# Kernel tuning notes

Measured on AMD Instinct MI355X. Metric: run time of the kernel, lower is better.

## Reference

```python
import jax, jax.numpy as jnp
import numpy as np

B = 256
N = 256


def setup_inputs() -> dict:
    key = jax.random.key(0)
    ks = jax.random.split(key, 6)
    X = jax.random.normal(ks[0], (B, N), dtype=jnp.float32)
    context = jax.random.normal(ks[1], (B, N), dtype=jnp.float32)
    W = jax.random.normal(ks[2], (N, N), dtype=jnp.float32) * 0.1
    scale = jnp.ones((1,), dtype=jnp.float32)
    A = jax.random.uniform(ks[3], (N, N), dtype=jnp.float32)
    cl_weight = jax.random.normal(ks[4], (N * N, N), dtype=jnp.float32) * 0.02
    cl_bias = jax.random.normal(ks[5], (N * N,), dtype=jnp.float32) * 0.02
    t = 3
    return {"X": X, "context": context, "W": W, "scale": scale, "A": A,
            "cl_weight": cl_weight, "cl_bias": cl_bias, "t": t}


def reference(X, context, W, scale, A, cl_weight, cl_bias, t):
    # context_L path: context-conditioned adjustment of W, shape [B, N, N]
    Bsz, n = X.shape
    adjust = (context @ cl_weight.T + cl_bias).reshape(Bsz, n, n)
    W_new = adjust + W  # broadcast [N,N] over batch
    # diag term: sum over rows i of (W_new @ A)[b, i, k] = einsum bij,jk->bk
    d = jnp.einsum('bij,jk->bk', W_new, A)
    eye = jnp.eye(n, dtype=X.dtype)
    L = d[:, :, None] * eye - W_new          # diag_embed(d) - W_new, [B,N,N]
    new_context = context * (t / (t + 1)) + X / (t + 1)
    L_T = scale * jnp.swapaxes(L, -1, -2)    # [B,N,N]
    update = jnp.einsum('bn,bnm->bm', X, L_T)  # matmul(X[...,None,:], L_T).squeeze()
    return (update, new_context)
```

## Files before the change

### kernel.cpp

```cpp
#include <hip/hip_runtime.h>

#define N 256
#define NN 65536

typedef __attribute__((ext_vector_type(8))) __bf16 bf16x8;
typedef __attribute__((ext_vector_type(4))) __bf16 bf16x4v;
typedef __attribute__((ext_vector_type(4))) float f32x4;

#define F_PART   0u
#define F_SPART  2097152u
#define F_WSC    2621440u
#define F_SFULL  2621696u
#define F_YADJ   2687232u
#define WS_FLOATS 2752768u

static __device__ __forceinline__ f32x4 mfma16(bf16x8 a, bf16x8 b, f32x4 c) {
  return __builtin_amdgcn_mfma_f32_16x16x32_bf16(a, b, c, 0, 0, 0);
}
static __device__ __forceinline__ bf16x4v pack4(float4 v) {
  bf16x4v r;
  r[0] = (__bf16)v.x; r[1] = (__bf16)v.y; r[2] = (__bf16)v.z; r[3] = (__bf16)v.w;
  return r;
}
static __device__ __forceinline__ bf16x8 pack8(float4 a, float4 b) {
  bf16x8 r;
  r[0] = (__bf16)a.x; r[1] = (__bf16)a.y; r[2] = (__bf16)a.z; r[3] = (__bf16)a.w;
  r[4] = (__bf16)b.x; r[5] = (__bf16)b.y; r[6] = (__bf16)b.z; r[7] = (__bf16)b.w;
  return r;
}

__global__ void __launch_bounds__(512) kbig(
    const float* __restrict__ X, const float* __restrict__ ctx,
    const float* __restrict__ W, const float* __restrict__ clb,
    const float* __restrict__ clw, float* __restrict__ ws)
{
  extern __shared__ char smem[];
  float* xl = (float*)(smem + 49152);
  const int t = threadIdx.x;
  const int mt = blockIdx.x >> 5, s = blockIdx.x & 31;
  const int n0 = s * 8, m0g = mt * 32;
  const float4* clwf4 = (const float4*)clw;

  int gm[4], gk[4];
  float4 gA[4], gB[4];
#pragma unroll
  for (int i = 0; i < 4; ++i) {
    const int idx = i * 512 + t;
    gm[i] = idx >> 6; gk[i] = idx & 63;
    gA[i] = clwf4[(m0g + gm[i]) * 16384 + (n0 + 0) * 64 + gk[i]];
  }
#pragma unroll
  for (int i = 0; i < 4; ++i)
    gB[i] = clwf4[(m0g + gm[i]) * 16384 + (n0 + 1) * 64 + gk[i]];

  const int lane = t & 63, w = t >> 6;
  const int wb = w * 32, l15 = lane & 15, lhi = lane >> 4;
  const int swz = (l15 & 7) << 4;

  bf16x8 af[2][8];
#pragma unroll
  for (int i = 0; i < 2; ++i)
#pragma unroll
    for (int c = 0; c < 8; ++c) {
      const float4* p =
          (const float4*)(ctx + (wb + i * 16 + l15) * N + c * 32 + lhi * 8);
      af[i][c] = pack8(p[0], p[1]);
    }

  if (t < 256) {
    const float4* xp = (const float4*)(X + t * N + n0);
    const float4 x0 = xp[0], x1 = xp[1];
    xl[0 * N + t] = x0.x; xl[1 * N + t] = x0.y; xl[2 * N + t] = x0.z; xl[3 * N + t] = x0.w;
    xl[4 * N + t] = x1.x; xl[5 * N + t] = x1.y; xl[6 * N + t] = x1.z; xl[7 * N + t] = x1.w;
  }
#pragma unroll
  for (int i = 0; i < 4; ++i)
    *(bf16x4v*)(smem + gm[i] * 512 + ((gk[i] * 8) ^ ((gm[i] & 7) << 4))) = pack4(gA[i]);
  __syncthreads();

  const f32x4 zero = {0.f, 0.f, 0.f, 0.f};
  f32x4 acc[2][2];
  acc[0][0] = zero; acc[0][1] = zero; acc[1][0] = zero; acc[1][1] = zero;

#pragma unroll
  for (int nn = 0; nn < 8; ++nn) {
    if (nn < 6) {
      if ((nn & 1) == 0) {
#pragma unroll
        for (int i = 0; i < 4; ++i)
          gA[i] = clwf4[(m0g + gm[i]) * 16384 + (n0 + nn + 2) * 64 + gk[i]];
      } else {
#pragma unroll
        for (int i = 0; i < 4; ++i)
          gB[i] = clwf4[(m0g + gm[i]) * 16384 + (n0 + nn + 2) * 64 + gk[i]];
      }
    }
    char* buf = smem + (nn % 3) * 16384;
    f32x4 h[2][2];
    h[0][0] = zero; h[0][1] = zero; h[1][0] = zero; h[1][1] = zero;
#pragma unroll
    for (int c = 0; c < 8; ++c) {
      const int kb = c * 64 + lhi * 16;
      bf16x8 b0 = *(const bf16x8*)(buf + l15 * 512 + (kb ^ swz));
      bf16x8 b1 = *(const bf16x8*)(buf + (16 + l15) * 512 + (kb ^ swz));
      h[0][0] = mfma16(af[0][c], b0, h[0][0]);
      h[0][1] = mfma16(af[0][c], b1, h[0][1]);
      h[1][0] = mfma16(af[1][c], b0, h[1][0]);
      h[1][1] = mfma16(af[1][c], b1, h[1][1]);
    }
    const int ng = n0 + nn;
#pragma unroll
    for (int fb = 0; fb < 2; ++fb) {
#pragma unroll
      for (int r = 0; r < 4; ++r) {
        const float xv = xl[nn * N + wb + fb * 16 + lhi * 4 + r];
        acc[fb][0][r] += xv * h[fb][0][r];
        acc[fb][1][r] += xv * h[fb][1][r];
        float v = h[fb][0][r] + h[fb][1][r];
        v += __shfl_xor(v, 1);
        v += __shfl_xor(v, 2);
        v += __shfl_xor(v, 4);
        v += __shfl_xor(v, 8);
        if (l15 == 0)
          ws[F_SPART + mt * NN + (wb + fb * 16 + lhi * 4 + r) * N + ng] = v;
      }
    }
    if (nn < 7) {
      char* nbuf = smem + ((nn + 1) % 3) * 16384;
      if (((nn + 1) & 1) == 0) {
#pragma unroll
        for (int i = 0; i < 4; ++i)
          *(bf16x4v*)(nbuf + gm[i] * 512 + ((gk[i] * 8) ^ ((gm[i] & 7) << 4))) = pack4(gA[i]);
      } else {
#pragma unroll
        for (int i = 0; i < 4; ++i)
          *(bf16x4v*)(nbuf + gm[i] * 512 + ((gk[i] * 8) ^ ((gm[i] & 7) << 4))) = pack4(gB[i]);
      }
    }
    __syncthreads();
  }
  const int base = blockIdx.x * 8192;
#pragma unroll
  for (int fb = 0; fb < 2; ++fb)
#pragma unroll
    for (int fm = 0; fm < 2; ++fm)
#pragma unroll
      for (int r = 0; r < 4; ++r)
        ws[F_PART + base + (wb + fb * 16 + lhi * 4 + r) * 32 + fm * 16 + l15] =
            acc[fb][fm][r];

  if (mt == 0) {
    float* red = xl;
    if (t < 256) {
      const float4* wp = (const float4*)(W + t * N + s * 8);
      const float4* cp = (const float4*)(clb + t * N + s * 8);
      const float4 a0 = wp[0], a1 = wp[1], b0 = cp[0], b1 = cp[1];
      red[0 * 256 + t] = a0.x + b0.x; red[1 * 256 + t] = a0.y + b0.y;
      red[2 * 256 + t] = a0.z + b0.z; red[3 * 256 + t] = a0.w + b0.w;
      red[4 * 256 + t] = a1.x + b1.x; red[5 * 256 + t] = a1.y + b1.y;
      red[6 * 256 + t] = a1.z + b1.z; red[7 * 256 + t] = a1.w + b1.w;
    }
    __syncthreads();
    if (t < 64) {
      const int jj = t >> 3, seg = t & 7;
      float v = 0.f;
#pragma unroll
      for (int i = 0; i < 32; ++i) v += red[jj * 256 + seg * 32 + i];
      v += __shfl_xor(v, 1);
      v += __shfl_xor(v, 2);
      v += __shfl_xor(v, 4);
      if (seg == 0) ws[F_WSC + s * 8 + jj] = v;
    }
  }
}

__global__ void __launch_bounds__(256) kred(float* __restrict__ ws)
{
  const int o = blockIdx.x * 256 + threadIdx.x;
  const int b = o >> 8, col = o & 255;
  const int mt = col >> 5, ml = col & 31;
  float y = 0.f;
#pragma unroll
  for (int si = 0; si < 32; ++si)
    y += ws[F_PART + ((mt * 32 + si) * 256 + b) * 32 + ml];
  ws[F_YADJ + o] = y;
  float sv = ws[F_WSC + col];
#pragma unroll
  for (int q = 0; q < 8; ++q)
    sv += ws[F_SPART + q * NN + o];
  ws[F_SFULL + o] = sv;
}

__global__ void __launch_bounds__(256) kfin(
    const float* __restrict__ X, const float* __restrict__ ctx,
    const float* __restrict__ W, const float* __restrict__ clb,
    const float* __restrict__ A, const float* __restrict__ scale,
    const int* __restrict__ tptr, float* __restrict__ out,
    float* __restrict__ ws)
{
  extern __shared__ char smem[];
  const int t = threadIdx.x, blk = blockIdx.x;
  const int b0 = (blk >> 3) * 32, k0 = (blk & 7) * 32;
  {
    const int row = t >> 3, q = t & 7;
    const int sw = (row & 7) << 4;
    const float4* sp = (const float4*)(ws + F_SFULL + (b0 + row) * N);
    const float4* xp = (const float4*)(X + (b0 + row) * N);
    const float4* wp = (const float4*)(W + (k0 + row) * N);
    const float4* cp = (const float4*)(clb + (k0 + row) * N);
#pragma unroll
    for (int i = 0; i < 8; ++i) {
      const int f4 = q * 8 + i;
      const int off = row * 512 + ((f4 * 8) ^ sw);
      *(bf16x4v*)(smem + off) = pack4(sp[f4]);
      *(bf16x4v*)(smem + 16384 + off) = pack4(xp[f4]);
      const float4 wv = wp[f4], cv = cp[f4];
      float4 s2;
      s2.x = wv.x + cv.x; s2.y = wv.y + cv.y;
      s2.z = wv.z + cv.z; s2.w = wv.w + cv.w;
      *(bf16x4v*)(smem + 49152 + off) = pack4(s2);
    }
    const float4* ap = (const float4*)(A + t * N + k0);
    char* at = smem + 32768;
#pragma unroll
    for (int i = 0; i < 8; ++i) {
      const float4 v = ap[i];
      const int kk = i * 4;
      *(__bf16*)(at + (kk + 0) * 512 + ((t * 2) ^ (((kk + 0) & 7) << 4))) = (__bf16)v.x;
      *(__bf16*)(at + (kk + 1) * 512 + ((t * 2) ^ (((kk + 1) & 7) << 4))) = (__bf16)v.y;
      *(__bf16*)(at + (kk + 2) * 512 + ((t * 2) ^ (((kk + 2) & 7) << 4))) = (__bf16)v.z;
      *(__bf16*)(at + (kk + 3) * 512 + ((t * 2) ^ (((kk + 3) & 7) << 4))) = (__bf16)v.w;
    }
  }
  __syncthreads();
  const int lane = t & 63, w = t >> 6;
  const int l15 = lane & 15, lhi = lane >> 4;
  const int wqb = (w >> 1) * 16, wqk = (w & 1) * 16;
  const int swz = (l15 & 7) << 4;
  f32x4 accd = {0.f, 0.f, 0.f, 0.f}, accw = {0.f, 0.f, 0.f, 0.f};
#pragma unroll
  for (int c = 0; c < 8; ++c) {
    const int kb = c * 64 + lhi * 16;
    bf16x8 as  = *(const bf16x8*)(smem + (wqb + l15) * 512 + (kb ^ swz));
    bf16x8 aat = *(const bf16x8*)(smem + 32768 + (wqk + l15) * 512 + (kb ^ swz));
    bf16x8 ax  = *(const bf16x8*)(smem + 16384 + (wqb + l15) * 512 + (kb ^ swz));
    bf16x8 awc = *(const bf16x8*)(smem + 49152 + (wqk + l15) * 512 + (kb ^ swz));
    accd = mfma16(as, aat, accd);
    accw = mfma16(ax, awc, accw);
  }
  const float sc = scale[0];
  const float tf = (float)(*tptr);
  const float c1 = tf / (tf + 1.f), c2 = 1.f / (tf + 1.f);
#pragma unroll
  for (int r = 0; r < 4; ++r) {
    const int b = b0 + wqb + lhi * 4 + r, k = k0 + wqk + l15;
    const int idx = b * N + k;
    const float xv = X[idx];
    out[idx] = sc * (xv * accd[r] - accw[r] - ws[F_YADJ + idx]);
    out[NN + idx] = ctx[idx] * c1 + xv * c2;
  }
}

extern "C" void kernel_launch(void* const* d_in, const int* in_sizes, int n_in,
                              void* d_out, int out_size, void* d_ws, size_t ws_size,
                              hipStream_t stream)
{
  (void)in_sizes; (void)n_in; (void)out_size;
  const float* X     = (const float*)d_in[0];
  const float* ctx   = (const float*)d_in[1];
  const float* W     = (const float*)d_in[2];
  const float* scale = (const float*)d_in[3];
  const float* A     = (const float*)d_in[4];
  const float* clw   = (const float*)d_in[5];
  const float* clb   = (const float*)d_in[6];
  const int*   tptr  = (const int*)d_in[7];
  float* out = (float*)d_out;
  float* ws  = (float*)d_ws;

  if (ws_size < (size_t)WS_FLOATS * sizeof(float)) return;

  (void)hipFuncSetAttribute((const void*)kbig,
                            hipFuncAttributeMaxDynamicSharedMemorySize, 57344);
  (void)hipFuncSetAttribute((const void*)kfin,
                            hipFuncAttributeMaxDynamicSharedMemorySize, 65536);

  kbig<<<256, 512, 57344, stream>>>(X, ctx, W, clb, clw, ws);
  kred<<<256, 256, 0, stream>>>(ws);
  kfin<<<64, 256, 65536, stream>>>(X, ctx, W, clb, A, scale, tptr, out, ws);
}
```

Baseline: 55.61 us.

## Deepen clw prefetch to three register stages and stage partial sums in LDS

Moves the global prefetch of cl_weight slices from two to three register buffers, so loads are issued three iterations ahead instead of two. The main loop is hand-unrolled via a macro, and the __syncthreads barriers become a raw s_barrier that only waits on LDS counters, so in-flight global loads are not drained at each step. Per-row scalar stores of the S partial sums now go to an LDS staging area and are written out once at the end as float4 stores. This raises register and LDS use (64KB dynamic shared), which may reduce occupancy.

New measurement: 53.73 us. -3.4%, faster.

```diff
diff --git a/kernel.cpp b/kernel.cpp
--- a/kernel.cpp
+++ b/kernel.cpp
@@ -28,6 +28,11 @@
   r[4] = (__bf16)b.x; r[5] = (__bf16)b.y; r[6] = (__bf16)b.z; r[7] = (__bf16)b.w;
   return r;
 }
+
+#define BAR()                                                  \
+  asm volatile("s_waitcnt lgkmcnt(0)" ::: "memory");           \
+  __builtin_amdgcn_s_barrier();                                \
+  __builtin_amdgcn_sched_barrier(0);
 
 __global__ void __launch_bounds__(512) kbig(
     const float* __restrict__ X, const float* __restrict__ ctx,
@@ -36,22 +41,26 @@
 {
   extern __shared__ char smem[];
   float* xl = (float*)(smem + 49152);
+  float* sred = (float*)(smem + 57344);
   const int t = threadIdx.x;
   const int mt = blockIdx.x >> 5, s = blockIdx.x & 31;
   const int n0 = s * 8, m0g = mt * 32;
   const float4* clwf4 = (const float4*)clw;
 
   int gm[4], gk[4];
-  float4 gA[4], gB[4];
+  float4 g0[4], g1[4], g2[4];
 #pragma unroll
   for (int i = 0; i < 4; ++i) {
     const int idx = i * 512 + t;
     gm[i] = idx >> 6; gk[i] = idx & 63;
-    gA[i] = clwf4[(m0g + gm[i]) * 16384 + (n0 + 0) * 64 + gk[i]];
+    g0[i] = clwf4[(m0g + gm[i]) * 16384 + (n0 + 0) * 64 + gk[i]];
   }
 #pragma unroll
   for (int i = 0; i < 4; ++i)
-    gB[i] = clwf4[(m0g + gm[i]) * 16384 + (n0 + 1) * 64 + gk[i]];
+    g1[i] = clwf4[(m0g + gm[i]) * 16384 + (n0 + 1) * 64 + gk[i]];
+#pragma unroll
+  for (int i = 0; i < 4; ++i)
+    g2[i] = clwf4[(m0g + gm[i]) * 16384 + (n0 + 2) * 64 + gk[i]];
 
   const int lane = t & 63, w = t >> 6;
   const int wb = w * 32, l15 = lane & 15, lhi = lane >> 4;
@@ -75,70 +84,67 @@
   }
 #pragma unroll
   for (int i = 0; i < 4; ++i)
-    *(bf16x4v*)(smem + gm[i] * 512 + ((gk[i] * 8) ^ ((gm[i] & 7) << 4))) = pack4(gA[i]);
-  __syncthreads();
+    *(bf16x4v*)(smem + gm[i] * 512 + ((gk[i] * 8) ^ ((gm[i] & 7) << 4))) = pack4(g0[i]);
+  BAR();
 
   const f32x4 zero = {0.f, 0.f, 0.f, 0.f};
   f32x4 acc[2][2];
   acc[0][0] = zero; acc[0][1] = zero; acc[1][0] = zero; acc[1][1] = zero;
 
-#pragma unroll
-  for (int nn = 0; nn < 8; ++nn) {
-    if (nn < 6) {
-      if ((nn & 1) == 0) {
-#pragma unroll
-        for (int i = 0; i < 4; ++i)
-          gA[i] = clwf4[(m0g + gm[i]) * 16384 + (n0 + nn + 2) * 64 + gk[i]];
-      } else {
-#pragma unroll
-        for (int i = 0; i < 4; ++i)
-          gB[i] = clwf4[(m0g + gm[i]) * 16384 + (n0 + nn + 2) * 64 + gk[i]];
-      }
-    }
-    char* buf = smem + (nn % 3) * 16384;
-    f32x4 h[2][2];
-    h[0][0] = zero; h[0][1] = zero; h[1][0] = zero; h[1][1] = zero;
-#pragma unroll
-    for (int c = 0; c < 8; ++c) {
-      const int kb = c * 64 + lhi * 16;
-      bf16x8 b0 = *(const bf16x8*)(buf + l15 * 512 + (kb ^ swz));
-      bf16x8 b1 = *(const bf16x8*)(buf + (16 + l15) * 512 + (kb ^ swz));
-      h[0][0] = mfma16(af[0][c], b0, h[0][0]);
-      h[0][1] = mfma16(af[0][c], b1, h[0][1]);
-      h[1][0] = mfma16(af[1][c], b0, h[1][0]);
-      h[1][1] = mfma16(af[1][c], b1, h[1][1]);
-    }
-    const int ng = n0 + nn;
-#pragma unroll
-    for (int fb = 0; fb < 2; ++fb) {
-#pragma unroll
-      for (int r = 0; r < 4; ++r) {
-        const float xv = xl[nn * N + wb + fb * 16 + lhi * 4 + r];
-        acc[fb][0][r] += xv * h[fb][0][r];
-        acc[fb][1][r] += xv * h[fb][1][r];
-        float v = h[fb][0][r] + h[fb][1][r];
-        v += __shfl_xor(v, 1);
-        v += __shfl_xor(v, 2);
-        v += __shfl_xor(v, 4);
-        v += __shfl_xor(v, 8);
-        if (l15 == 0)
-          ws[F_SPART + mt * NN + (wb + fb * 16 + lhi * 4 + r) * N + ng] = v;
-      }
-    }
-    if (nn < 7) {
-      char* nbuf = smem + ((nn + 1) % 3) * 16384;
-      if (((nn + 1) & 1) == 0) {
-#pragma unroll
-        for (int i = 0; i < 4; ++i)
-          *(bf16x4v*)(nbuf + gm[i] * 512 + ((gk[i] * 8) ^ ((gm[i] & 7) << 4))) = pack4(gA[i]);
-      } else {
-#pragma unroll
-        for (int i = 0; i < 4; ++i)
-          *(bf16x4v*)(nbuf + gm[i] * 512 + ((gk[i] * 8) ^ ((gm[i] & 7) << 4))) = pack4(gB[i]);
-      }
-    }
-    __syncthreads();
-  }
+#define KITER(NN, DO_ISSUE, GISS, DO_WRITE, GWR)                              \
+  {                                                                           \
+    if (DO_ISSUE) {                                                           \
+      _Pragma("unroll")                                                       \
+      for (int i = 0; i < 4; ++i)                                             \
+        GISS[i] = clwf4[(m0g + gm[i]) * 16384 + (n0 + (NN) + 3) * 64 + gk[i]];\
+    }                                                                         \
+    char* buf = smem + ((NN) % 3) * 16384;                                    \
+    f32x4 h[2][2];                                                            \
+    h[0][0] = zero; h[0][1] = zero; h[1][0] = zero; h[1][1] = zero;           \
+    _Pragma("unroll")                                                         \
+    for (int c = 0; c < 8; ++c) {                                             \
+      const int kb = c * 64 + lhi * 16;                                       \
+      bf16x8 b0 = *(const bf16x8*)(buf + l15 * 512 + (kb ^ swz));             \
+      bf16x8 b1 = *(const bf16x8*)(buf + (16 + l15) * 512 + (kb ^ swz));      \
+      h[0][0] = mfma16(af[0][c], b0, h[0][0]);                                \
+      h[0][1] = mfma16(af[0][c], b1, h[0][1]);                                \
+      h[1][0] = mfma16(af[1][c], b0, h[1][0]);                                \
+      h[1][1] = mfma16(af[1][c], b1, h[1][1]);                                \
+    }                                                                         \
+    _Pragma("unroll")                                                         \
+    for (int fb = 0; fb < 2; ++fb) {                                          \
+      _Pragma("unroll")                                                       \
+      for (int r = 0; r < 4; ++r) {                                           \
+        const int brow = wb + fb * 16 + lhi * 4 + r;                          \
+        const float xv = xl[(NN) * N + brow];                                 \
+        acc[fb][0][r] += xv * h[fb][0][r];                                    \
+        acc[fb][1][r] += xv * h[fb][1][r];                                    \
+        float v = h[fb][0][r] + h[fb][1][r];                                  \
+        v += __shfl_xor(v, 1); v += __shfl_xor(v, 2);                         \
+        v += __shfl_xor(v, 4); v += __shfl_xor(v, 8);                         \
+        if (l15 == 0) sred[(NN) * 256 + brow] = v;                            \
+      }                                                                       \
+    }                                                                         \
+    if (DO_WRITE) {                                                           \
+      char* wbuf = smem + (((NN) + 1) % 3) * 16384;                           \
+      _Pragma("unroll")                                                       \
+      for (int i = 0; i < 4; ++i)                                             \
+        *(bf16x4v*)(wbuf + gm[i] * 512 +                                      \
+                    ((gk[i] * 8) ^ ((gm[i] & 7) << 4))) = pack4(GWR[i]);      \
+    }                                                                         \
+    BAR();                                                                    \
+  }
+
+  KITER(0, 1, g0, 1, g1)
+  KITER(1, 1, g1, 1, g2)
+  KITER(2, 1, g2, 1, g0)
+  KITER(3, 1, g0, 1, g1)
+  KITER(4, 1, g1, 1, g2)
+  KITER(5, 0, g0, 1, g0)
+  KITER(6, 0, g0, 1, g1)
+  KITER(7, 0, g0, 0, g0)
+#undef KITER
+
   const int base = blockIdx.x * 8192;
 #pragma unroll
   for (int fb = 0; fb < 2; ++fb)
@@ -149,7 +155,19 @@
         ws[F_PART + base + (wb + fb * 16 + lhi * 4 + r) * 32 + fm * 16 + l15] =
             acc[fb][fm][r];
 
+  {
+    const int b = wb + (lane >> 1);
+    const int nh = (lane & 1) * 4;
+    float4 v;
+    v.x = sred[(nh + 0) * 256 + b];
+    v.y = sred[(nh + 1) * 256 + b];
+    v.z = sred[(nh + 2) * 256 + b];
+    v.w = sred[(nh + 3) * 256 + b];
+    *(float4*)(ws + F_SPART + mt * NN + b * N + n0 + nh) = v;
+  }
+
   if (mt == 0) {
+    __syncthreads();
     float* red = xl;
     if (t < 256) {
       const float4* wp = (const float4*)(W + t * N + s * 8);
@@ -280,11 +298,11 @@
   if (ws_size < (size_t)WS_FLOATS * sizeof(float)) return;
 
   (void)hipFuncSetAttribute((const void*)kbig,
-                            hipFuncAttributeMaxDynamicSharedMemorySize, 57344);
+                            hipFuncAttributeMaxDynamicSharedMemorySize, 65536);
   (void)hipFuncSetAttribute((const void*)kfin,
                             hipFuncAttributeMaxDynamicSharedMemorySize, 65536);
 
-  kbig<<<256, 512, 57344, stream>>>(X, ctx, W, clb, clw, ws);
+  kbig<<<256, 512, 65536, stream>>>(X, ctx, W, clb, clw, ws);
   kred<<<256, 256, 0, stream>>>(ws);
   kfin<<<64, 256, 65536, stream>>>(X, ctx, W, clb, A, scale, tptr, out, ws);
 }
```
